# Kernel optimization log

Hardware: AMD Instinct MI355X
Metric: run time of the kernel (lower is better)

The kernel has to match this reference:

```python
import jax, jax.numpy as jnp
import numpy as np

K = 9          # kernel_size (number of KNN neighbours), dilation=1
SCALAR = 20.0  # scalar in _build_explain
EPS = 1e-10


def setup_inputs() -> dict:
    key = jax.random.key(0)
    ks = jax.random.split(key, 9)
    B, C, H, W = 16, 192, 28, 28
    Cout, r = 384, 16
    f = lambda k, s, sc: jax.random.normal(k, s, jnp.float32) * sc
    return {
        "x": f(ks[0], (B, C, H, W), 1.0),
        "w_edge": f(ks[1], (Cout, 2 * C), 0.05),  # 1x1 conv on concat[x_i, x_j-x_i]
        "b_edge": f(ks[2], (Cout,), 0.05),
        "w1": f(ks[3], (C // r, C), 0.1),          # CBAM channel MLP (shared)
        "b1": f(ks[4], (C // r,), 0.1),
        "w2": f(ks[5], (C, C // r), 0.1),
        "b2": f(ks[6], (C,), 0.1),
        "w_sp": f(ks[7], (1, 2, 7, 7), 0.1),       # CBAM spatial 7x7 conv
        "b_sp": f(ks[8], (1,), 0.1),
    }


def _cbam(x, w1, b1, w2, b2, w_sp, b_sp):
    # Standard CBAM: channel gate (avg+max pooled -> shared MLP -> sigmoid)
    # then spatial gate (channel mean/max -> 7x7 conv -> sigmoid).
    mlp = lambda v: jax.nn.relu(v @ w1.T + b1) @ w2.T + b2
    ch = jax.nn.sigmoid(mlp(x.mean((2, 3))) + mlp(x.max((2, 3))))
    x = x * ch[:, :, None, None]
    sp_in = jnp.stack([x.mean(1), x.max(1)], axis=1)  # (B,2,H,W)
    sp = jax.lax.conv_general_dilated(sp_in, w_sp, (1, 1), [(3, 3), (3, 3)])
    return x * jax.nn.sigmoid(sp + b_sp[None, :, None, None])


def _build_explain(att_x):
    B, C, H, W = att_x.shape
    a = jax.nn.softmax(att_x.reshape(B, C, H * W), axis=2)
    a = a / (a.max(axis=2, keepdims=True) + EPS)
    return (2.0 * a - 1.0) / (2.0 * SCALAR) + 1.0  # (B,C,N)


def _knn_idx(xf):
    # DenseDilatedKnnGraph: L2-normalize over channels, pairwise sq-dist, topk.
    xn = xf / jnp.maximum(jnp.linalg.norm(xf, axis=1, keepdims=True), 1e-12)
    xt = jnp.swapaxes(xn, 1, 2)                      # (B,N,C)
    sq = jnp.sum(xt * xt, axis=-1)                   # (B,N)
    dist = sq[:, :, None] - 2.0 * jnp.einsum("bnc,bmc->bnm", xt, xt) + sq[:, None, :]
    _, idx = jax.lax.top_k(-dist, K)                 # nn_idx = edge_index[0], (B,N,K)
    return idx


def reference(x, w_edge, b_edge, w1, b1, w2, b2, w_sp, b_sp):
    B, C, H, W = x.shape
    N = H * W
    xf = x.reshape(B, C, N)
    idx = _knn_idx(xf)                               # dynamic KNN graph (B,N,K)
    att = _build_explain(_cbam(x, w1, b1, w2, b2, w_sp, b_sp))
    xf = xf * att
    # EdgeConv2d: x_i = center (edge_index[1] is arange -> broadcast),
    # x_j gathered by neighbour indices.
    x_i = xf[:, :, :, None]                           # (B,C,N,1)
    x_e = jnp.broadcast_to(x_i, (B, C, N, K))
    i_e = jnp.broadcast_to(idx[:, None, :, :], (B, C, N, K))
    x_j = jnp.take_along_axis(x_e, i_e, axis=2)       # (B,C,N,K)
    feat = jnp.concatenate([x_e, x_j - x_i], axis=1)  # (B,2C,N,K)
    out = jnp.einsum("oc,bcnk->bonk", w_edge, feat) + b_edge[None, :, None, None]
    out = jax.nn.relu(out)                            # BasicConv: 1x1 conv + relu
    out = out.max(axis=-1)                            # max over neighbours (B,O,N)
    return out.reshape(B, -1, H, W)
```

## Files before the change

kernel.cpp:

```cpp
#include <hip/hip_runtime.h>
#include <math.h>

#define HW 784
#define Cc 192
#define Bb 16
#define CO 384
#define KK 9
#define OG 8

typedef __attribute__((ext_vector_type(8))) short bf16x8;
typedef __attribute__((ext_vector_type(4))) float f32x4;

__device__ __forceinline__ unsigned f2ord(float f){
  unsigned u = __float_as_uint(f);
  return (u & 0x80000000u) ? ~u : (u | 0x80000000u);
}

__device__ __forceinline__ unsigned short b16rne(float v){
  unsigned u = __float_as_uint(v);
  unsigned r = u + 0x7FFFu + ((u >> 16) & 1u);
  return (unsigned short)(r >> 16);
}

__global__ void k_chstats(const float* __restrict__ x, float* __restrict__ chm, float* __restrict__ chx){
  int wid = threadIdx.x >> 6, lane = threadIdx.x & 63;
  int r = blockIdx.x * 4 + wid;
  const float4* row = (const float4*)(x + (size_t)r * HW);
  float s = 0.f, m = -3.4e38f;
  #pragma unroll
  for (int i = 0; i < 4; ++i){
    int f4 = lane + 64*i;
    if (f4 < 196){
      float4 v = row[f4];
      s += v.x + v.y + v.z + v.w;
      m = fmaxf(m, fmaxf(fmaxf(v.x, v.y), fmaxf(v.z, v.w)));
    }
  }
  for (int off = 32; off; off >>= 1){ s += __shfl_xor(s, off); m = fmaxf(m, __shfl_xor(m, off)); }
  if (lane == 0){ chm[r] = s / (float)HW; chx[r] = m; }
}

__global__ void k_mlp(const float* __restrict__ chm, const float* __restrict__ chx,
                      const float* __restrict__ w1, const float* __restrict__ b1,
                      const float* __restrict__ w2, const float* __restrict__ b2,
                      float* __restrict__ chv){
  int b = blockIdx.x, t = threadIdx.x;
  __shared__ float vm[Cc], vx[Cc], hp[2][12];
  if (t < Cc){ vm[t] = chm[b*Cc + t]; vx[t] = chx[b*Cc + t]; }
  __syncthreads();
  if (t < 24){
    int h = t % 12;
    const float* src = (t < 12) ? vm : vx;
    float a = b1[h];
    for (int c = 0; c < Cc; ++c) a += src[c] * w1[h*Cc + c];
    hp[t/12][h] = fmaxf(a, 0.f);
  }
  __syncthreads();
  if (t < Cc){
    float a = 2.f * b2[t];
    for (int h = 0; h < 12; ++h) a += (hp[0][h] + hp[1][h]) * w2[t*12 + h];
    chv[b*Cc + t] = 1.f / (1.f + expf(-a));
  }
}

__global__ void k_spin(const float* __restrict__ x, const float* __restrict__ chv,
                       float* __restrict__ amean, float* __restrict__ amax,
                       float* __restrict__ nrm){
  int b = blockIdx.x >> 2;
  int n = ((blockIdx.x & 3) << 8) + threadIdx.x;
  if (n >= HW) return;
  const float* xb = x + (size_t)b*Cc*HW + n;
  const float* cb = chv + b*Cc;
  float s = 0.f, m = -3.4e38f, sq = 0.f;
  for (int c = 0; c < Cc; ++c){
    float xv = xb[(size_t)c*HW];
    float v = xv * cb[c];
    s += v; m = fmaxf(m, v); sq += xv*xv;
  }
  amean[b*HW + n] = s / (float)Cc;
  amax[b*HW + n]  = m;
  nrm[b*HW + n]   = fmaxf(sqrtf(sq), 1e-12f);
}

__global__ void k_conv(const float* __restrict__ amean, const float* __restrict__ amax,
                       const float* __restrict__ wsp, const float* __restrict__ bsp,
                       float* __restrict__ satt){
  int b = blockIdx.x >> 2;
  int n = ((blockIdx.x & 3) << 8) + threadIdx.x;
  if (n >= HW) return;
  int yy = n / 28, xx = n % 28;
  float a = 0.f;
  for (int ky = 0; ky < 7; ++ky){
    int iy = yy + ky - 3; if (iy < 0 || iy >= 28) continue;
    for (int kx = 0; kx < 7; ++kx){
      int ix = xx + kx - 3; if (ix < 0 || ix >= 28) continue;
      int ii = b*HW + iy*28 + ix;
      a += amean[ii]*wsp[ky*7 + kx] + amax[ii]*wsp[49 + ky*7 + kx];
    }
  }
  satt[b*HW + n] = 1.f / (1.f + expf(-(a + bsp[0])));
}

__global__ void k_attstats(const float* __restrict__ x, const float* __restrict__ chv,
                           const float* __restrict__ satt,
                           float* __restrict__ vmaxA, float* __restrict__ invA){
  int wid = threadIdx.x >> 6, lane = threadIdx.x & 63;
  int r = blockIdx.x * 4 + wid;
  int b = r / Cc;
  const float4* row = (const float4*)(x + (size_t)r * HW);
  const float4* sr  = (const float4*)(satt + b * HW);
  float ch = chv[r];
  float4 vv[4];
  float m = -3.4e38f;
  #pragma unroll
  for (int i = 0; i < 4; ++i){
    int f4 = lane + 64*i;
    if (f4 < 196){
      float4 xv = row[f4], sv = sr[f4];
      vv[i].x = (xv.x * ch) * sv.x; vv[i].y = (xv.y * ch) * sv.y;
      vv[i].z = (xv.z * ch) * sv.z; vv[i].w = (xv.w * ch) * sv.w;
      m = fmaxf(m, fmaxf(fmaxf(vv[i].x, vv[i].y), fmaxf(vv[i].z, vv[i].w)));
    }
  }
  for (int off = 32; off; off >>= 1) m = fmaxf(m, __shfl_xor(m, off));
  float s = 0.f;
  #pragma unroll
  for (int i = 0; i < 4; ++i){
    int f4 = lane + 64*i;
    if (f4 < 196){
      s += expf(vv[i].x - m) + expf(vv[i].y - m) + expf(vv[i].z - m) + expf(vv[i].w - m);
    }
  }
  for (int off = 32; off; off >>= 1) s += __shfl_xor(s, off);
  if (lane == 0){ vmaxA[r] = m; invA[r] = 1.f / (1.f + 1e-10f * s); }
}

__global__ __launch_bounds__(256) void k_cvt2wp(const float* __restrict__ x, const float* __restrict__ nrm,
                                                const float* __restrict__ chv, const float* __restrict__ satt,
                                                const float* __restrict__ vmaxA, const float* __restrict__ invA,
                                                const float* __restrict__ we,
                                                unsigned short* __restrict__ Xnh, unsigned short* __restrict__ Xnl,
                                                unsigned short* __restrict__ XAh, unsigned short* __restrict__ XAl,
                                                unsigned short* __restrict__ Wph, unsigned short* __restrict__ Wpl){
  int bid = blockIdx.x, t = threadIdx.x;
  if (bid >= 624){
    int i = (bid - 624)*256 + t;
    int o = i / Cc, c = i % Cc;
    float v = (o < CO) ? (we[(size_t)o*384 + c] - we[(size_t)o*384 + Cc + c])
                       : we[(size_t)(o - CO)*384 + Cc + c];
    unsigned short h = b16rne(v);
    float lo = v - __uint_as_float((unsigned)h << 16);
    Wph[i] = h;
    Wpl[i] = b16rne(lo);
    return;
  }
  int xx = bid % 13, yy = (bid / 13) % 3, b = bid / 39;
  int c0 = yy*64, n0 = xx*64;
  __shared__ float T[64][65];
  __shared__ float chs[64], vms[64], ivs[64];
  int nl = (t & 15) * 4, cl = t >> 4;
  const float* xb = x + (size_t)b*Cc*HW;
  #pragma unroll
  for (int r = 0; r < 4; ++r){
    int c_loc = cl + r*16;
    int n = n0 + nl;
    float4 v = (n < HW) ? *(const float4*)(xb + (size_t)(c0 + c_loc)*HW + n) : make_float4(0,0,0,0);
    *(float4*)&T[c_loc][nl] = v;
  }
  if (t < 64){
    chs[t] = chv[b*Cc + c0 + t];
    vms[t] = vmaxA[b*Cc + c0 + t];
    ivs[t] = invA[b*Cc + c0 + t];
  }
  __syncthreads();
  int nr = t >> 2, q = t & 3;
  int n_g = n0 + nr;
  if (n_g >= HW) return;
  float nv = nrm[b*HW + n_g];
  float sr = satt[b*HW + n_g];
  unsigned int nh[8], nlw[8], ah[8], al[8];
  #pragma unroll
  for (int j = 0; j < 8; ++j){
    unsigned int parts[2][2];
    #pragma unroll
    for (int e = 0; e < 2; ++e){
      int cc_ = q*16 + 2*j + e;
      float v = T[cc_][nr];
      float xnv = v / nv;
      unsigned short h0 = b16rne(xnv);
      float l0 = xnv - __uint_as_float((unsigned)h0 << 16);
      parts[0][e] = (unsigned)h0 | ((unsigned)b16rne(l0) << 16);
      float vvv = (v * chs[cc_]) * sr;
      float ex = expf(vvv - vms[cc_]);
      float a = ex * ivs[cc_];
      float xav = v * ((2.f*a - 1.f)*0.025f + 1.f);
      unsigned short h1 = b16rne(xav);
      float l1 = xav - __uint_as_float((unsigned)h1 << 16);
      parts[1][e] = (unsigned)h1 | ((unsigned)b16rne(l1) << 16);
    }
    nh[j]  = (parts[0][0] & 0xFFFFu) | (parts[0][1] << 16);
    nlw[j] = (parts[0][0] >> 16)     | (parts[0][1] & 0xFFFF0000u);
    ah[j]  = (parts[1][0] & 0xFFFFu) | (parts[1][1] << 16);
    al[j]  = (parts[1][0] >> 16)     | (parts[1][1] & 0xFFFF0000u);
  }
  size_t base = ((size_t)b*HW + n_g)*Cc + c0 + q*16;
  *(uint4*)(Xnh + base)     = make_uint4(nh[0], nh[1], nh[2], nh[3]);
  *(uint4*)(Xnh + base + 8) = make_uint4(nh[4], nh[5], nh[6], nh[7]);
  *(uint4*)(Xnl + base)     = make_uint4(nlw[0], nlw[1], nlw[2], nlw[3]);
  *(uint4*)(Xnl + base + 8) = make_uint4(nlw[4], nlw[5], nlw[6], nlw[7]);
  *(uint4*)(XAh + base)     = make_uint4(ah[0], ah[1], ah[2], ah[3]);
  *(uint4*)(XAh + base + 8) = make_uint4(ah[4], ah[5], ah[6], ah[7]);
  *(uint4*)(XAl + base)     = make_uint4(al[0], al[1], al[2], al[3]);
  *(uint4*)(XAl + base + 8) = make_uint4(al[4], al[5], al[6], al[7]);
}

__global__ __launch_bounds__(256) void k_gramgemm(const unsigned short* __restrict__ Xnh,
                                                  const unsigned short* __restrict__ Xnl,
                                                  const unsigned short* __restrict__ Wph,
                                                  const unsigned short* __restrict__ Wpl,
                                                  const unsigned short* __restrict__ XAh,
                                                  const unsigned short* __restrict__ XAl,
                                                  float* __restrict__ D, float* __restrict__ PQ){
  __shared__ unsigned short Als[8192];
  __shared__ unsigned short Bls[8192];
  int bid = blockIdx.x;
  int t = threadIdx.x, w = t >> 6, l = t & 63;
  int wr = w >> 1, wc = w & 1;
  f32x4 acc[4][4] = {};
  int nn = t >> 1, half = t & 1;

  bool isGram = bid < 784;
  int b, r0, c0;
  const unsigned short *A_h, *A_l, *B_h, *B_l;
  if (isGram){
    b = bid / 49; int rem = bid % 49;
    c0 = (rem % 7) * 128; r0 = (rem / 7) * 128;
    size_t bb = (size_t)b*HW*Cc;
    A_h = Xnh + bb; A_l = Xnl + bb; B_h = Xnh + bb; B_l = Xnl + bb;
  } else {
    int id = bid - 784;
    b = id / 42; int rem = id % 42;
    c0 = (rem % 7) * 128; r0 = (rem / 7) * 128;
    size_t bb = (size_t)b*HW*Cc;
    A_h = Wph; A_l = Wpl; B_h = XAh + bb; B_l = XAl + bb;
  }
  int ra = r0 + nn; if (isGram && ra > HW-1) ra = HW-1;
  int rb = c0 + nn; if (rb > HW-1) rb = HW-1;

  for (int cc = 0; cc < 9; ++cc){
    int seg = cc/3, kc0 = (cc%3)*64;
    const unsigned short* As_ = (seg < 2 ? A_h : A_l);
    const unsigned short* Bs_ = (seg == 1 ? B_l : B_h);
    const uint4* ga = (const uint4*)(As_ + (size_t)ra*Cc + kc0 + half*32);
    const uint4* gb = (const uint4*)(Bs_ + (size_t)rb*Cc + kc0 + half*32);
    uint4 va0 = ga[0], va1 = ga[1], va2 = ga[2], va3 = ga[3];
    uint4 vb0 = gb[0], vb1 = gb[1], vb2 = gb[2], vb3 = gb[3];
    __syncthreads();
    int base = nn*128 + half*64;
    int sw = (nn & 7) << 4;
    *(uint4*)((char*)Als + ((base      ) ^ sw)) = va0;
    *(uint4*)((char*)Als + ((base + 16 ) ^ sw)) = va1;
    *(uint4*)((char*)Als + ((base + 32 ) ^ sw)) = va2;
    *(uint4*)((char*)Als + ((base + 48 ) ^ sw)) = va3;
    *(uint4*)((char*)Bls + ((base      ) ^ sw)) = vb0;
    *(uint4*)((char*)Bls + ((base + 16 ) ^ sw)) = vb1;
    *(uint4*)((char*)Bls + ((base + 32 ) ^ sw)) = vb2;
    *(uint4*)((char*)Bls + ((base + 48 ) ^ sw)) = vb3;
    __syncthreads();
    #pragma unroll
    for (int ks = 0; ks < 2; ++ks){
      bf16x8 af[4], bfr[4];
      int kb = ks*64 + (l >> 4)*16;
      #pragma unroll
      for (int mt = 0; mt < 4; ++mt){
        int rl = wr*64 + mt*16 + (l & 15);
        int off = (rl*128 + kb) ^ ((rl & 7) << 4);
        af[mt] = *(const bf16x8*)((const char*)Als + off);
      }
      #pragma unroll
      for (int nt = 0; nt < 4; ++nt){
        int cl2 = wc*64 + nt*16 + (l & 15);
        int off = (cl2*128 + kb) ^ ((cl2 & 7) << 4);
        bfr[nt] = *(const bf16x8*)((const char*)Bls + off);
      }
      #pragma unroll
      for (int mt = 0; mt < 4; ++mt)
        #pragma unroll
        for (int nt = 0; nt < 4; ++nt)
          acc[mt][nt] = __builtin_amdgcn_mfma_f32_16x16x32_bf16(af[mt], bfr[nt], acc[mt][nt], 0, 0, 0);
    }
  }
  if (isGram){
    #pragma unroll
    for (int mt = 0; mt < 4; ++mt){
      #pragma unroll
      for (int nt = 0; nt < 4; ++nt){
        int col = c0 + wc*64 + nt*16 + (l & 15);
        if (col >= HW) continue;
        int row0 = r0 + wr*64 + mt*16 + ((l >> 4) << 2);
        #pragma unroll
        for (int r = 0; r < 4; ++r){
          int row = row0 + r;
          if (row < HW) D[((size_t)b*HW + row)*HW + col] = -acc[mt][nt][r];
        }
      }
    }
  } else {
    #pragma unroll
    for (int mt = 0; mt < 4; ++mt){
      #pragma unroll
      for (int nt = 0; nt < 4; ++nt){
        int col = c0 + wc*64 + nt*16 + (l & 15);
        if (col >= HW) continue;
        int row0 = r0 + wr*64 + mt*16 + ((l >> 4) << 2);
        #pragma unroll
        for (int r = 0; r < 4; ++r){
          PQ[((size_t)b*768 + row0 + r)*HW + col] = acc[mt][nt][r];
        }
      }
    }
  }
}

__global__ __launch_bounds__(256) void k_select(const float* __restrict__ D, int* __restrict__ idxo){
  int wid = threadIdx.x >> 6, lane = threadIdx.x & 63;
  int row = blockIdx.x * 4 + wid;
  const float* Dr = D + (size_t)row * HW;
  float dvv[13]; int mvv[13];
  #pragma unroll
  for (int i = 0; i < 13; ++i){
    int m = lane + 64*i;
    dvv[i] = (m < HW) ? Dr[m] : 3.4e38f;
    mvv[i] = m;
  }
  for (int k = 0; k < KK; ++k){
    float bd = dvv[0]; int bi = 0;
    #pragma unroll
    for (int i = 1; i < 13; ++i) if (dvv[i] < bd){ bd = dvv[i]; bi = i; }
    unsigned long long key = ((unsigned long long)f2ord(bd) << 32) | (unsigned)mvv[bi];
    for (int off = 32; off; off >>= 1){
      unsigned long long o = __shfl_xor(key, off);
      if (o < key) key = o;
    }
    int wm = (int)(unsigned)(key & 0xffffffffu);
    if (lane == 0) idxo[(size_t)k*(Bb*HW) + row] = wm;
    if (mvv[bi] == wm) dvv[bi] = 3.4e38f;
  }
}

__global__ __launch_bounds__(256) void k_edge(const float* __restrict__ PQ, const int* __restrict__ idx,
                                              const float* __restrict__ be, float* __restrict__ out){
  int bid = blockIdx.x;
  int b = bid / (CO/OG), og = bid % (CO/OG);
  int o0 = og * OG;
  __shared__ float Qls[OG][HW + 4];
  const float* Qbase = PQ + ((size_t)b*768 + CO + o0)*HW;
  int t = threadIdx.x;
  #pragma unroll
  for (int oo = 0; oo < OG; ++oo){
    if (t < 196) *(float4*)&Qls[oo][t*4] = *(const float4*)(Qbase + (size_t)oo*HW + t*4);
  }
  __syncthreads();
  const float* Pbase = PQ + ((size_t)b*768 + o0)*HW;
  float bev[OG];
  #pragma unroll
  for (int oo = 0; oo < OG; ++oo) bev[oo] = be[o0 + oo];
  for (int n = t; n < HW; n += 256){
    int ip[KK];
    #pragma unroll
    for (int k = 0; k < KK; ++k) ip[k] = idx[(size_t)k*(Bb*HW) + b*HW + n];
    float qm[OG];
    #pragma unroll
    for (int oo = 0; oo < OG; ++oo) qm[oo] = -3.4e38f;
    #pragma unroll
    for (int k = 0; k < KK; ++k){
      int j = ip[k];
      #pragma unroll
      for (int oo = 0; oo < OG; ++oo) qm[oo] = fmaxf(qm[oo], Qls[oo][j]);
    }
    #pragma unroll
    for (int oo = 0; oo < OG; ++oo){
      out[((size_t)b*CO + o0 + oo)*HW + n] = fmaxf(Pbase[(size_t)oo*HW + n] + bev[oo] + qm[oo], 0.f);
    }
  }
}

extern "C" void kernel_launch(void* const* d_in, const int* in_sizes, int n_in,
                              void* d_out, int out_size, void* d_ws, size_t ws_size,
                              hipStream_t stream){
  const float* x   = (const float*)d_in[0];
  const float* we  = (const float*)d_in[1];
  const float* be  = (const float*)d_in[2];
  const float* w1  = (const float*)d_in[3];
  const float* b1  = (const float*)d_in[4];
  const float* w2  = (const float*)d_in[5];
  const float* b2  = (const float*)d_in[6];
  const float* wsp = (const float*)d_in[7];
  const float* bsp = (const float*)d_in[8];
  float* out = (float*)d_out;

  float* ws    = (float*)d_ws;
  float* chm   = ws;
  float* chx   = chm + 3072;
  float* chv   = chx + 3072;
  float* vmaxA = chv + 3072;
  float* invA  = vmaxA + 3072;
  float* amean = invA + 3072;
  float* amax  = amean + 12544;
  float* satt  = amax + 12544;
  float* nrm   = satt + 12544;
  unsigned short* Wph = (unsigned short*)(nrm + 12544);
  unsigned short* Wpl = Wph + 147456;
  unsigned short* Xnh = Wpl + 147456;
  unsigned short* Xnl = Xnh + 2408448;
  unsigned short* XAh = Xnl + 2408448;
  unsigned short* XAl = XAh + 2408448;
  int*   idx   = (int*)(XAl + 2408448);
  float* D     = (float*)(idx + 112896);
  float* PQ    = D + 9834496;

  k_chstats<<<768, 256, 0, stream>>>(x, chm, chx);
  k_mlp<<<16, 192, 0, stream>>>(chm, chx, w1, b1, w2, b2, chv);
  k_spin<<<64, 256, 0, stream>>>(x, chv, amean, amax, nrm);
  k_conv<<<64, 256, 0, stream>>>(amean, amax, wsp, bsp, satt);
  k_attstats<<<768, 256, 0, stream>>>(x, chv, satt, vmaxA, invA);
  k_cvt2wp<<<1200, 256, 0, stream>>>(x, nrm, chv, satt, vmaxA, invA, we,
                                     Xnh, Xnl, XAh, XAl, Wph, Wpl);
  k_gramgemm<<<1456, 256, 0, stream>>>(Xnh, Xnl, Wph, Wpl, XAh, XAl, D, PQ);
  k_select<<<3136, 256, 0, stream>>>(D, idx);
  k_edge<<<Bb*(CO/OG), 256, 0, stream>>>(PQ, idx, be, out);
}
```

Before: 146.0 us.

## Exploit Gram matrix symmetry and remap block ids across XCDs

The pairwise-distance Gram GEMM now computes only the upper-triangular 128x128 tiles per batch, 28 instead of 49. Each off-diagonal tile also writes its transpose, staging it through shared memory so the mirrored rows go out as coalesced float4 stores. This is meant to cut roughly 40% of the Gram MFMA work and its operand loads. Block ids are also permuted by a stride-8 mapping, apparently to group neighbouring tiles on the same XCD for better L2 reuse. The cost is extra LDS traffic and barriers in the epilogue, plus uneven work between diagonal and off-diagonal blocks.

```diff
diff --git a/kernel.cpp b/kernel.cpp
--- a/kernel.cpp
+++ b/kernel.cpp
@@ -221,24 +221,35 @@
                                                   const unsigned short* __restrict__ XAh,
                                                   const unsigned short* __restrict__ XAl,
                                                   float* __restrict__ D, float* __restrict__ PQ){
-  __shared__ unsigned short Als[8192];
-  __shared__ unsigned short Bls[8192];
-  int bid = blockIdx.x;
+  __shared__ __align__(16) char smem[32768];
+  unsigned short* Als = (unsigned short*)smem;
+  unsigned short* Bls = Als + 8192;
+  float* Tt = (float*)smem;
+
+  int hwbid = blockIdx.x;
+  int bid = (hwbid & 7) * 140 + (hwbid >> 3);
   int t = threadIdx.x, w = t >> 6, l = t & 63;
   int wr = w >> 1, wc = w & 1;
   f32x4 acc[4][4] = {};
   int nn = t >> 1, half = t & 1;
 
-  bool isGram = bid < 784;
-  int b, r0, c0;
+  bool isGram = bid < 448;
+  int b, r0, c0, ty = 0, tx = 0;
   const unsigned short *A_h, *A_l, *B_h, *B_l;
   if (isGram){
-    b = bid / 49; int rem = bid % 49;
-    c0 = (rem % 7) * 128; r0 = (rem / 7) * 128;
+    b = bid / 28; int rm = bid % 28;
+    if      (rm <  7){ ty=0; tx=rm; }
+    else if (rm < 13){ ty=1; tx=1+rm-7; }
+    else if (rm < 18){ ty=2; tx=2+rm-13; }
+    else if (rm < 22){ ty=3; tx=3+rm-18; }
+    else if (rm < 25){ ty=4; tx=4+rm-22; }
+    else if (rm < 27){ ty=5; tx=5+rm-25; }
+    else             { ty=6; tx=6; }
+    r0 = ty*128; c0 = tx*128;
     size_t bb = (size_t)b*HW*Cc;
     A_h = Xnh + bb; A_l = Xnl + bb; B_h = Xnh + bb; B_l = Xnl + bb;
   } else {
-    int id = bid - 784;
+    int id = bid - 448;
     b = id / 42; int rem = id % 42;
     c0 = (rem % 7) * 128; r0 = (rem / 7) * 128;
     size_t bb = (size_t)b*HW*Cc;
@@ -305,6 +316,34 @@
         }
       }
     }
+    if (tx > ty){
+      #pragma unroll
+      for (int nt = 0; nt < 4; ++nt){
+        __syncthreads();
+        int ci = wc*16 + (l & 15);
+        #pragma unroll
+        for (int mt = 0; mt < 4; ++mt){
+          int row = wr*64 + mt*16 + ((l >> 4) << 2);
+          #pragma unroll
+          for (int r = 0; r < 4; ++r)
+            Tt[ci*129 + row + r] = -acc[mt][nt][r];
+        }
+        __syncthreads();
+        int ci2 = t >> 3;
+        int col = c0 + (ci2 >> 4)*64 + nt*16 + (ci2 & 15);
+        if (col < HW){
+          float* Drow = D + ((size_t)b*HW + col)*HW + r0;
+          int rbase = (t & 7)*16;
+          #pragma unroll
+          for (int j = 0; j < 4; ++j){
+            int rr = rbase + j*4;
+            float4 v = make_float4(Tt[ci2*129 + rr],     Tt[ci2*129 + rr + 1],
+                                   Tt[ci2*129 + rr + 2], Tt[ci2*129 + rr + 3]);
+            *(float4*)(Drow + rr) = v;
+          }
+        }
+      }
+    }
   } else {
     #pragma unroll
     for (int mt = 0; mt < 4; ++mt){
@@ -426,7 +465,7 @@
   k_attstats<<<768, 256, 0, stream>>>(x, chv, satt, vmaxA, invA);
   k_cvt2wp<<<1200, 256, 0, stream>>>(x, nrm, chv, satt, vmaxA, invA, we,
                                      Xnh, Xnl, XAh, XAl, Wph, Wpl);
-  k_gramgemm<<<1456, 256, 0, stream>>>(Xnh, Xnl, Wph, Wpl, XAh, XAl, D, PQ);
+  k_gramgemm<<<1120, 256, 0, stream>>>(Xnh, Xnl, Wph, Wpl, XAh, XAl, D, PQ);
   k_select<<<3136, 256, 0, stream>>>(D, idx);
   k_edge<<<Bb*(CO/OG), 256, 0, stream>>>(PQ, idx, be, out);
 }
```

New measurement: 142.6 us. 2.3% less time.
